# Optimization experiments

Measured on AMD Instinct MI355X. Metric: run time of the kernel, lower is better.

The kernel has to match this reference:

```python
import jax, jax.numpy as jnp
import numpy as np

N_EMBD = 1024
N_HEAD = 16
HEAD_SIZE = N_EMBD // N_HEAD
BLOCK_SIZE = 2048
B, T = 2, 2048
EPS = 1e-5


def _layernorm(x, g, b):
    mu = jnp.mean(x, axis=-1, keepdims=True)
    var = jnp.mean(jnp.square(x - mu), axis=-1, keepdims=True)
    return (x - mu) * jax.lax.rsqrt(var + EPS) * g + b


def setup_inputs() -> dict:
    key = jax.random.key(0)
    ks = jax.random.split(key, 12)
    s = 0.02
    x = jax.random.normal(ks[0], (B, T, N_EMBD), dtype=jnp.float32)
    wq = jax.random.normal(ks[1], (N_HEAD, N_EMBD, HEAD_SIZE), jnp.float32) * s
    wk = jax.random.normal(ks[2], (N_HEAD, N_EMBD, HEAD_SIZE), jnp.float32) * s
    wv = jax.random.normal(ks[3], (N_HEAD, N_EMBD, HEAD_SIZE), jnp.float32) * s
    w_proj = jax.random.normal(ks[4], (N_EMBD, N_EMBD), jnp.float32) * s
    b_proj = jnp.zeros((N_EMBD,), jnp.float32)
    w1 = jax.random.normal(ks[5], (N_EMBD, 4 * N_EMBD), jnp.float32) * s
    b1 = jnp.zeros((4 * N_EMBD,), jnp.float32)
    w2 = jax.random.normal(ks[6], (4 * N_EMBD, N_EMBD), jnp.float32) * s
    b2 = jnp.zeros((N_EMBD,), jnp.float32)
    g1 = jnp.ones((N_EMBD,), jnp.float32)
    be1 = jnp.zeros((N_EMBD,), jnp.float32)
    g2 = jnp.ones((N_EMBD,), jnp.float32)
    be2 = jnp.zeros((N_EMBD,), jnp.float32)
    return dict(x=x, wq=wq, wk=wk, wv=wv, w_proj=w_proj, b_proj=b_proj,
                w1=w1, b1=b1, w2=w2, b2=b2, g1=g1, be1=be1, g2=g2, be2=be2)


def reference(x, wq, wk, wv, w_proj, b_proj, w1, b1, w2, b2, g1, be1, g2, be2):
    # --- self-attention with pre-LN ---
    h = _layernorm(x, g1, be1)
    q = jnp.einsum('btc,hcd->bhtd', h, wq)
    k = jnp.einsum('btc,hcd->bhtd', h, wk)
    v = jnp.einsum('btc,hcd->bhtd', h, wv)
    scores = jnp.einsum('bhtd,bhsd->bhts', q, k) / np.sqrt(HEAD_SIZE).astype(np.float32)
    causal = jnp.tril(jnp.ones((T, T), dtype=bool))
    scores = jnp.where(causal, scores, -jnp.inf)
    weights = jax.nn.softmax(scores, axis=-1)
    attn = jnp.einsum('bhts,bhsd->bhtd', weights, v)  # (B,H,T,D)
    attn = attn.transpose(0, 2, 1, 3).reshape(B, T, N_EMBD)  # concat heads
    sa = attn @ w_proj + b_proj
    x = x + sa
    # --- feed-forward with pre-LN ---
    h2 = _layernorm(x, g2, be2)
    ff = jax.nn.relu(h2 @ w1 + b1) @ w2 + b2
    return x + ff
```

## Files before the change

kernel.cpp:

```cpp
#include <hip/hip_runtime.h>
#include <hip/hip_bf16.h>
#include <cstdint>


typedef unsigned short u16;
typedef __attribute__((ext_vector_type(8))) __bf16 bf16x8;
typedef __attribute__((ext_vector_type(4))) float f32x4;

__device__ __forceinline__ float b2f(u16 v) {
    union { float f; unsigned int u; } x; x.u = ((unsigned int)v) << 16; return x.f;
}
__device__ __forceinline__ u16 f2b(float f) {
    union { float f; unsigned int u; } x; x.f = f;
    unsigned int u = x.u;
    u += 0x7fffu + ((u >> 16) & 1u);
    return (u16)(u >> 16);
}

__device__ __forceinline__ f32x4 mfma16(bf16x8 a, bf16x8 b, f32x4 c) {
    return __builtin_amdgcn_mfma_f32_16x16x32_bf16(a, b, c, 0, 0, 0);
}

__device__ __forceinline__ void load_lds16(const u16* g, u16* l) {
    __builtin_amdgcn_global_load_lds(
        (const __attribute__((address_space(1))) unsigned int*)g,
        (__attribute__((address_space(3))) unsigned int*)l, 16, 0, 0);
}

__global__ __launch_bounds__(256) void transpose_all(
    const float* __restrict__ wq, const float* __restrict__ wk,
    const float* __restrict__ wv, const float* __restrict__ wp,
    const float* __restrict__ w1, const float* __restrict__ w2,
    u16* __restrict__ wqkvt, u16* __restrict__ wpt,
    u16* __restrict__ w1t, u16* __restrict__ w2t)
{
    __shared__ float tile[32][33];
    int id = blockIdx.x;
    const float* src; u16* dst; int R, C, bx, by;
    if (id < 3072) {
        const int m = id >> 10;
        src = (m == 0) ? wq : (m == 1) ? wk : wv;
        dst = wqkvt + m * 1048576u;
        int t = id & 1023;
        const int b = t >> 6; t &= 63;
        R = 1024; C = 64; bx = t & 1; by = t >> 1;
        src += (size_t)b * 65536; dst += (size_t)b * 65536;
    } else if (id < 4096) {
        int t = id - 3072; src = wp; dst = wpt;
        R = 1024; C = 1024; bx = t & 31; by = t >> 5;
    } else if (id < 8192) {
        int t = id - 4096; src = w1; dst = w1t;
        R = 1024; C = 4096; bx = t & 127; by = t >> 7;
    } else {
        int t = id - 8192; src = w2; dst = w2t;
        R = 4096; C = 1024; bx = t & 31; by = t >> 5;
    }
    const int tx = threadIdx.x, ty = threadIdx.y;
    const int c0 = bx * 32, r0 = by * 32;
#pragma unroll
    for (int i = 0; i < 4; ++i) {
        int r = ty * 4 + i;
        tile[r][tx] = src[(size_t)(r0 + r) * C + c0 + tx];
    }
    __syncthreads();
#pragma unroll
    for (int i = 0; i < 4; ++i) {
        int r = ty * 4 + i;
        dst[(size_t)(c0 + r) * R + r0 + tx] = f2b(tile[tx][r]);
    }
}

__global__ __launch_bounds__(256) void ln_kernel(
    const float* __restrict__ x, const float* __restrict__ g,
    const float* __restrict__ be, u16* __restrict__ out)
{
    const int row = blockIdx.x;
    const int tid = threadIdx.x;
    const float* xr = x + (size_t)row * 1024;
    float v[4];
#pragma unroll
    for (int i = 0; i < 4; ++i) v[i] = xr[tid + i * 256];
    float s = v[0] + v[1] + v[2] + v[3];
    float q = v[0]*v[0] + v[1]*v[1] + v[2]*v[2] + v[3]*v[3];
#pragma unroll
    for (int o = 1; o < 64; o <<= 1) {
        s += __shfl_xor(s, o, 64);
        q += __shfl_xor(q, o, 64);
    }
    __shared__ float red[8];
    const int wave = tid >> 6;
    if ((tid & 63) == 0) { red[wave] = s; red[4 + wave] = q; }
    __syncthreads();
    s = red[0] + red[1] + red[2] + red[3];
    q = red[4] + red[5] + red[6] + red[7];
    const float mu = s * (1.0f / 1024.0f);
    const float var = q * (1.0f / 1024.0f) - mu * mu;
    const float rstd = rsqrtf(var + 1e-5f);
#pragma unroll
    for (int i = 0; i < 4; ++i) {
        int idx = tid + i * 256;
        out[(size_t)row * 1024 + idx] = f2b((v[i] - mu) * rstd * g[idx] + be[idx]);
    }
}

template <int EPI, int TM, int TN, int WM, int WN>
__global__ __launch_bounds__(256, 2) void gemm_bt(
    const u16* __restrict__ A, const u16* __restrict__ Bt,
    int M, int N, int K,
    const float* __restrict__ bias, const float* __restrict__ resid_f,
    u16* __restrict__ out_b, float* __restrict__ out_f)
{
    constexpr int MI = WM / 16, NI = WN / 16;
    constexpr int MWAVES = TM / WM;
    __shared__ alignas(16) u16 As[TM * 64];
    __shared__ alignas(16) u16 Bs[TN * 64];
    const int tid = threadIdx.x;
    const int wave = tid >> 6, lane = tid & 63;
    const int lr = lane >> 4, lc = lane & 15;
    const int m0 = blockIdx.x * TM, n0 = blockIdx.y * TN;
    const int wm = (wave % MWAVES) * WM, wn = (wave / MWAVES) * WN;

    f32x4 acc[MI][NI];
#pragma unroll
    for (int i = 0; i < MI; ++i)
#pragma unroll
        for (int j = 0; j < NI; ++j) acc[i][j] = (f32x4){0.f, 0.f, 0.f, 0.f};

    const int srow = lane >> 3;
    const int skb = (lane & 7) ^ srow;
    const u16* Agp = A + (size_t)(m0 + wave * 8 + srow) * K + skb * 8;
    const u16* Bgp = Bt + (size_t)(n0 + wave * 8 + srow) * K + skb * 8;
    const int ldst = wave * 512;

    for (int k0 = 0; k0 < K; k0 += 64) {
#pragma unroll
        for (int i = 0; i < TM / 32; ++i)
            load_lds16(Agp + (size_t)i * 32 * K + k0, As + i * 2048 + ldst);
#pragma unroll
        for (int i = 0; i < TN / 32; ++i)
            load_lds16(Bgp + (size_t)i * 32 * K + k0, Bs + i * 2048 + ldst);
        __syncthreads();
#pragma unroll
        for (int h = 0; h < 2; ++h) {
            const int qh = ((h * 4 + lr) ^ (lc & 7)) * 8;
            bf16x8 af[MI], bfr[NI];
#pragma unroll
            for (int i = 0; i < MI; ++i)
                af[i] = *(const bf16x8*)&As[(wm + i * 16 + lc) * 64 + qh];
#pragma unroll
            for (int j = 0; j < NI; ++j)
                bfr[j] = *(const bf16x8*)&Bs[(wn + j * 16 + lc) * 64 + qh];
#pragma unroll
            for (int i = 0; i < MI; ++i)
#pragma unroll
                for (int j = 0; j < NI; ++j)
                    acc[i][j] = mfma16(af[i], bfr[j], acc[i][j]);
        }
        __syncthreads();
    }

#pragma unroll
    for (int i = 0; i < MI; ++i) {
#pragma unroll
        for (int j = 0; j < NI; ++j) {
#pragma unroll
            for (int r = 0; r < 4; ++r) {
                const int m = m0 + wm + i * 16 + lr * 4 + r;
                const int n = n0 + wn + j * 16 + lc;
                const float v = acc[i][j][r];
                if (EPI == 0) {
                    const int group = n >> 10, nn = n & 1023;
                    const int hh = nn >> 6, dd = nn & 63;
                    const int bb = m >> 11, tt = m & 2047;
                    if (group == 0)
                        out_b[(((size_t)(bb * 16 + hh) * 2048) + tt) * 64 + dd] =
                            f2b(v * 0.125f);
                    else if (group == 1)
                        out_b[4194304u + (((size_t)(bb * 16 + hh) * 2048) + tt) * 64 + dd] =
                            f2b(v);
                    else
                        out_b[8388608u + (((size_t)(bb * 16 + hh) * 64) + dd) * 2048 + tt] =
                            f2b(v);
                } else if (EPI == 4) {
                    size_t idx = (size_t)m * N + n;
                    float rv = v + bias[n];
                    out_b[idx] = f2b(rv > 0.f ? rv : 0.f);
                } else {
                    size_t idx = (size_t)m * N + n;
                    out_f[idx] = resid_f[idx] + v + bias[n];
                }
            }
        }
    }
}

__global__ __launch_bounds__(256) void attn_kernel(
    const u16* __restrict__ qb, const u16* __restrict__ kb,
    const u16* __restrict__ vtb, u16* __restrict__ ob)
{
    const int bh = blockIdx.y;
    const int b = bh >> 4, h = bh & 15;
    const int tid = threadIdx.x, wave = tid >> 6, lane = tid & 63;
    const int lr = lane >> 4, lc = lane & 15;
    const int qx = lc & 7;
    __shared__ alignas(16) u16 Ks[64 * 64];
    __shared__ alignas(16) u16 Vts[64 * 64];
    __shared__ alignas(16) u16 Ps[4][16 * 64];
    const size_t base = (size_t)bh * (2048 * 64);

    const int srow = lane >> 3;
    const int sdb = (lane & 7) ^ srow;
    const u16* kg0 = kb + base + (size_t)(wave * 16 + srow) * 64 + sdb * 8;
    const u16* vg0 = vtb + base + (size_t)(wave * 16 + srow) * 2048 + sdb * 8;
    u16* KsW = Ks + wave * 16 * 64;
    u16* VsW = Vts + wave * 16 * 64;
    const int q0 = (lr ^ qx) * 8;
    const int q1 = ((4 + lr) ^ qx) * 8;

    for (int half = 0; half < 2; ++half) {
        const int qt = half ? (31 - (int)blockIdx.x) : (int)blockIdx.x;
        const int t0 = qt * 64;
        const int trow = t0 + wave * 16 + lc;
        const bf16x8 qf0 = *(const bf16x8*)&qb[base + (size_t)trow * 64 + lr * 8];
        const bf16x8 qf1 = *(const bf16x8*)&qb[base + (size_t)trow * 64 + 32 + lr * 8];
        f32x4 O[4];
        float pls[4];
#pragma unroll
        for (int j = 0; j < 4; ++j) O[j] = (f32x4){0.f, 0.f, 0.f, 0.f};
#pragma unroll
        for (int r = 0; r < 4; ++r) pls[r] = 0.f;

        for (int c = 0; c <= qt; ++c) {
            const int s0 = c * 64;
            load_lds16(kg0 + (size_t)s0 * 64, KsW);
            load_lds16(kg0 + (size_t)s0 * 64 + 512, KsW + 512);
            load_lds16(vg0 + s0, VsW);
            load_lds16(vg0 + s0 + 8 * 2048, VsW + 512);
            __syncthreads();

            f32x4 sc[4];
#pragma unroll
            for (int j = 0; j < 4; ++j) sc[j] = (f32x4){0.f, 0.f, 0.f, 0.f};
#pragma unroll
            for (int j = 0; j < 4; ++j) {
                const int row = (j * 16 + lc) * 64;
                bf16x8 k0 = *(const bf16x8*)&Ks[row + q0];
                bf16x8 k1 = *(const bf16x8*)&Ks[row + q1];
                sc[j] = mfma16(qf0, k0, sc[j]);
                sc[j] = mfma16(qf1, k1, sc[j]);
            }
            const bool diag = (c == qt);
#pragma unroll
            for (int r = 0; r < 4; ++r) {
                const int tl = lr * 4 + r;
#pragma unroll
                for (int j = 0; j < 4; ++j) {
                    float pv = __expf(sc[j][r]);
                    if (diag && (j * 16 + lc > wave * 16 + tl)) pv = 0.f;
                    pls[r] += pv;
                    const int sb = j * 2 + (lc >> 3);
                    Ps[wave][tl * 64 + ((sb ^ (tl & 7)) * 8) + (lc & 7)] = f2b(pv);
                }
            }
            const bf16x8 pf0 = *(const bf16x8*)&Ps[wave][lc * 64 + q0];
            const bf16x8 pf1 = *(const bf16x8*)&Ps[wave][lc * 64 + q1];
#pragma unroll
            for (int j = 0; j < 4; ++j) {
                const int row = (j * 16 + lc) * 64;
                bf16x8 v0 = *(const bf16x8*)&Vts[row + q0];
                bf16x8 v1 = *(const bf16x8*)&Vts[row + q1];
                O[j] = mfma16(pf0, v0, O[j]);
                O[j] = mfma16(pf1, v1, O[j]);
            }
            __syncthreads();
        }

        float linv[4];
#pragma unroll
        for (int r = 0; r < 4; ++r) {
            float l = pls[r];
            l += __shfl_xor(l, 1, 64);
            l += __shfl_xor(l, 2, 64);
            l += __shfl_xor(l, 4, 64);
            l += __shfl_xor(l, 8, 64);
            linv[r] = 1.0f / l;
        }
#pragma unroll
        for (int j = 0; j < 4; ++j)
#pragma unroll
            for (int r = 0; r < 4; ++r) {
                const int tr = t0 + wave * 16 + lr * 4 + r;
                ob[((size_t)b * 2048 + tr) * 1024 + h * 64 + j * 16 + lc] =
                    f2b(O[j][r] * linv[r]);
            }
    }
}

extern "C" void kernel_launch(void* const* d_in, const int* in_sizes, int n_in,
                              void* d_out, int out_size, void* d_ws, size_t ws_size,
                              hipStream_t stream)
{
    (void)in_sizes; (void)n_in; (void)out_size; (void)ws_size;
    const float* x   = (const float*)d_in[0];
    const float* wq  = (const float*)d_in[1];
    const float* wk  = (const float*)d_in[2];
    const float* wv  = (const float*)d_in[3];
    const float* wp  = (const float*)d_in[4];
    const float* bp  = (const float*)d_in[5];
    const float* w1  = (const float*)d_in[6];
    const float* b1  = (const float*)d_in[7];
    const float* w2  = (const float*)d_in[8];
    const float* b2  = (const float*)d_in[9];
    const float* g1  = (const float*)d_in[10];
    const float* be1 = (const float*)d_in[11];
    const float* g2  = (const float*)d_in[12];
    const float* be2 = (const float*)d_in[13];
    float* out = (float*)d_out;

    char* ws = (char*)d_ws;
    const size_t MB = 1024ull * 1024;
    u16*   h1    = (u16*)(ws + 0);
    u16*   wqkvt = (u16*)(ws + 8 * MB);
    u16*   wpt   = (u16*)(ws + 14 * MB);
    u16*   w1t   = (u16*)(ws + 16 * MB);
    u16*   w2t   = (u16*)(ws + 24 * MB);
    u16*   qkv   = (u16*)(ws + 32 * MB);
    u16*   attnb = (u16*)(ws + 56 * MB);
    u16*   ff1   = (u16*)(ws + 32 * MB);
    float* x2    = (float*)(ws + 64 * MB);
    u16*   h2    = h1;
    u16*   qb    = qkv;
    u16*   kbf   = qkv + 4194304u;
    u16*   vtb   = qkv + 8388608u;

    transpose_all<<<12288, dim3(32, 8), 0, stream>>>(
        wq, wk, wv, wp, w1, w2, wqkvt, wpt, w1t, w2t);

    ln_kernel<<<4096, 256, 0, stream>>>(x, g1, be1, h1);

    gemm_bt<0, 128, 128, 64, 64><<<dim3(32, 24), 256, 0, stream>>>(
        h1, wqkvt, 4096, 3072, 1024, nullptr, nullptr, qkv, nullptr);

    attn_kernel<<<dim3(16, 32), 256, 0, stream>>>(qb, kbf, vtb, attnb);

    gemm_bt<3, 64, 128, 32, 64><<<dim3(64, 8), 256, 0, stream>>>(
        attnb, wpt, 4096, 1024, 1024, bp, x, nullptr, x2);

    ln_kernel<<<4096, 256, 0, stream>>>(x2, g2, be2, h2);

    gemm_bt<4, 128, 128, 64, 64><<<dim3(32, 32), 256, 0, stream>>>(
        h2, w1t, 4096, 4096, 1024, b1, nullptr, ff1, nullptr);

    gemm_bt<5, 64, 128, 32, 64><<<dim3(64, 8), 256, 0, stream>>>(
        ff1, w2t, 4096, 1024, 4096, b2, x2, nullptr, out);
}
```

Baseline: 340.1 us.

## Deepen K tile for narrow GEMMs and remap attention blocks per XCD

Adds a BK template parameter so the 64x128 projection and FFN2 GEMMs stage 128 K-elements per barrier pair, halving the synchronizations per K sweep at the cost of doubled LDS use per block. The attention launch becomes a flat 1D grid, with block index decoded so each XCD gets the same (batch,head) groups, aiming to improve L2 locality of K/V across the chiplets. Also swaps the manual bf16 rounding for the intrinsic conversion.

```diff
diff --git a/kernel.cpp b/kernel.cpp
--- a/kernel.cpp
+++ b/kernel.cpp
@@ -7,14 +7,8 @@
 typedef __attribute__((ext_vector_type(8))) __bf16 bf16x8;
 typedef __attribute__((ext_vector_type(4))) float f32x4;
 
-__device__ __forceinline__ float b2f(u16 v) {
-    union { float f; unsigned int u; } x; x.u = ((unsigned int)v) << 16; return x.f;
-}
 __device__ __forceinline__ u16 f2b(float f) {
-    union { float f; unsigned int u; } x; x.f = f;
-    unsigned int u = x.u;
-    u += 0x7fffu + ((u >> 16) & 1u);
-    return (u16)(u >> 16);
+    return __builtin_bit_cast(unsigned short, __float2bfloat16(f));
 }
 
 __device__ __forceinline__ f32x4 mfma16(bf16x8 a, bf16x8 b, f32x4 c) {
@@ -103,7 +97,7 @@
     }
 }
 
-template <int EPI, int TM, int TN, int WM, int WN>
+template <int EPI, int TM, int TN, int WM, int WN, int BK>
 __global__ __launch_bounds__(256, 2) void gemm_bt(
     const u16* __restrict__ A, const u16* __restrict__ Bt,
     int M, int N, int K,
@@ -112,8 +106,9 @@
 {
     constexpr int MI = WM / 16, NI = WN / 16;
     constexpr int MWAVES = TM / WM;
-    __shared__ alignas(16) u16 As[TM * 64];
-    __shared__ alignas(16) u16 Bs[TN * 64];
+    constexpr int SS = BK / 64;
+    __shared__ alignas(16) u16 As[TM * BK];
+    __shared__ alignas(16) u16 Bs[TN * BK];
     const int tid = threadIdx.x;
     const int wave = tid >> 6, lane = tid & 63;
     const int lr = lane >> 4, lc = lane & 15;
@@ -132,24 +127,30 @@
     const u16* Bgp = Bt + (size_t)(n0 + wave * 8 + srow) * K + skb * 8;
     const int ldst = wave * 512;
 
-    for (int k0 = 0; k0 < K; k0 += 64) {
-#pragma unroll
-        for (int i = 0; i < TM / 32; ++i)
-            load_lds16(Agp + (size_t)i * 32 * K + k0, As + i * 2048 + ldst);
-#pragma unroll
-        for (int i = 0; i < TN / 32; ++i)
-            load_lds16(Bgp + (size_t)i * 32 * K + k0, Bs + i * 2048 + ldst);
+    for (int k0 = 0; k0 < K; k0 += BK) {
+#pragma unroll
+        for (int s = 0; s < SS; ++s) {
+#pragma unroll
+            for (int i = 0; i < TM / 32; ++i)
+                load_lds16(Agp + (size_t)i * 32 * K + k0 + s * 64,
+                           As + s * TM * 64 + i * 2048 + ldst);
+#pragma unroll
+            for (int i = 0; i < TN / 32; ++i)
+                load_lds16(Bgp + (size_t)i * 32 * K + k0 + s * 64,
+                           Bs + s * TN * 64 + i * 2048 + ldst);
+        }
         __syncthreads();
 #pragma unroll
-        for (int h = 0; h < 2; ++h) {
-            const int qh = ((h * 4 + lr) ^ (lc & 7)) * 8;
+        for (int h = 0; h < BK / 32; ++h) {
+            const int ss = h >> 1, hh = h & 1;
+            const int qh = ((hh * 4 + lr) ^ (lc & 7)) * 8;
             bf16x8 af[MI], bfr[NI];
 #pragma unroll
             for (int i = 0; i < MI; ++i)
-                af[i] = *(const bf16x8*)&As[(wm + i * 16 + lc) * 64 + qh];
+                af[i] = *(const bf16x8*)&As[ss * TM * 64 + (wm + i * 16 + lc) * 64 + qh];
 #pragma unroll
             for (int j = 0; j < NI; ++j)
-                bfr[j] = *(const bf16x8*)&Bs[(wn + j * 16 + lc) * 64 + qh];
+                bfr[j] = *(const bf16x8*)&Bs[ss * TN * 64 + (wn + j * 16 + lc) * 64 + qh];
 #pragma unroll
             for (int i = 0; i < MI; ++i)
 #pragma unroll
@@ -198,7 +199,10 @@
     const u16* __restrict__ qb, const u16* __restrict__ kb,
     const u16* __restrict__ vtb, u16* __restrict__ ob)
 {
-    const int bh = blockIdx.y;
+    const int id = blockIdx.x;
+    const int xcd = id & 7;
+    const int xq = (id >> 3) & 15;
+    const int bh = (id >> 7) * 8 + xcd;
     const int b = bh >> 4, h = bh & 15;
     const int tid = threadIdx.x, wave = tid >> 6, lane = tid & 63;
     const int lr = lane >> 4, lc = lane & 15;
@@ -218,7 +222,7 @@
     const int q1 = ((4 + lr) ^ qx) * 8;
 
     for (int half = 0; half < 2; ++half) {
-        const int qt = half ? (31 - (int)blockIdx.x) : (int)blockIdx.x;
+        const int qt = half ? (31 - xq) : xq;
         const int t0 = qt * 64;
         const int trow = t0 + wave * 16 + lc;
         const bf16x8 qf0 = *(const bf16x8*)&qb[base + (size_t)trow * 64 + lr * 8];
@@ -338,19 +342,19 @@
 
     ln_kernel<<<4096, 256, 0, stream>>>(x, g1, be1, h1);
 
-    gemm_bt<0, 128, 128, 64, 64><<<dim3(32, 24), 256, 0, stream>>>(
+    gemm_bt<0, 128, 128, 64, 64, 64><<<dim3(32, 24), 256, 0, stream>>>(
         h1, wqkvt, 4096, 3072, 1024, nullptr, nullptr, qkv, nullptr);
 
-    attn_kernel<<<dim3(16, 32), 256, 0, stream>>>(qb, kbf, vtb, attnb);
-
-    gemm_bt<3, 64, 128, 32, 64><<<dim3(64, 8), 256, 0, stream>>>(
+    attn_kernel<<<512, 256, 0, stream>>>(qb, kbf, vtb, attnb);
+
+    gemm_bt<3, 64, 128, 32, 64, 128><<<dim3(64, 8), 256, 0, stream>>>(
         attnb, wpt, 4096, 1024, 1024, bp, x, nullptr, x2);
 
     ln_kernel<<<4096, 256, 0, stream>>>(x2, g2, be2, h2);
 
-    gemm_bt<4, 128, 128, 64, 64><<<dim3(32, 32), 256, 0, stream>>>(
+    gemm_bt<4, 128, 128, 64, 64, 64><<<dim3(32, 32), 256, 0, stream>>>(
         h2, w1t, 4096, 4096, 1024, b1, nullptr, ff1, nullptr);
 
-    gemm_bt<5, 64, 128, 32, 64><<<dim3(64, 8), 256, 0, stream>>>(
+    gemm_bt<5, 64, 128, 32, 64, 128><<<dim3(64, 8), 256, 0, stream>>>(
         ff1, w2t, 4096, 1024, 4096, b2, x2, nullptr, out);
 }
```

Measured after the change: 305.7 us. 10.1% less time.
